# Kernel optimization log

Measured on AMD Instinct MI355X. Metric: run time of the kernel, lower is better.

The kernel has to match this reference:

```python
import jax, jax.numpy as jnp
import numpy as np

B, F, D, K = 4096, 1, 256, 65536

def setup_inputs() -> dict:
    key = jax.random.key(0)
    k1, k2, k3 = jax.random.split(key, 3)
    xhat_BFD = jax.random.normal(k1, (B, F, D), dtype=jnp.float32)
    x_BD = jax.random.normal(k2, (B * F, D), dtype=jnp.float32)
    centroids = jax.random.normal(k3, (K, D), dtype=jnp.float32)
    return {"xhat_BFD": xhat_BFD, "x_BD": x_BD, "centroids": centroids}

def reference(xhat_BFD, x_BD, centroids):
    c_sq_K = jnp.sum(centroids * centroids, axis=-1)            # [K]
    dists_BK = c_sq_K[None, :] - 2.0 * (x_BD @ centroids.T)     # [B*F, K] (GEMM-based distances)
    codes_B = jnp.argmin(dists_BK, axis=-1)                      # [B*F]
    quant_x_BD = centroids[codes_B]                              # embedding lookup of winners
    Bb, Ff, Dd = xhat_BFD.shape
    xhat_next = quant_x_BD.reshape(Bb, Ff, Dd)
    codes_BF = codes_B.reshape(Bb, Ff)
    return xhat_next, codes_BF
```

## Files before the change

kernel.cpp:

```cpp
#include <hip/hip_runtime.h>
#include <hip/hip_bf16.h>
#include <math.h>


#define DDIM 256
#define QTILE 128
#define STSZ 4096
#define QCAP 48
#define F16_MINN 6.103515625e-5f

typedef __attribute__((ext_vector_type(8))) _Float16 half8;
typedef __attribute__((ext_vector_type(4))) _Float16 half4;
typedef __attribute__((ext_vector_type(4))) float f32x4;

__device__ __forceinline__ void gl_lds16(const void* g, void* l) {
  __builtin_amdgcn_global_load_lds((const __attribute__((address_space(1))) void*)g,
                                   (__attribute__((address_space(3))) void*)l, 16, 0, 0);
}

__device__ __forceinline__ unsigned fkey(float d) {
  unsigned ud = __float_as_uint(d);
  return ud ^ (((int)ud < 0) ? 0xFFFFFFFFu : 0x80000000u);
}

__global__ void initctl_kernel(unsigned* __restrict__ ctl) {
  if (threadIdx.x < 64) ctl[threadIdx.x] = 0u;
}

__global__ __launch_bounds__(256) void splitc_kernel(const float* __restrict__ in,
                                                     _Float16* __restrict__ o0,
                                                     float* __restrict__ c_sq) {
  int i = blockIdx.x * 256 + threadIdx.x;
  int lane = (int)threadIdx.x & 63;
  float4 v = ((const float4*)in)[i];
  float vv[4] = {v.x, v.y, v.z, v.w};
  half4 h0;
#pragma unroll
  for (int e = 0; e < 4; ++e)
    h0[e] = (fabsf(vv[e]) < F16_MINN) ? (_Float16)0.f : (_Float16)vv[e];
  *(half4*)(o0 + (size_t)i * 4) = h0;
  float s = fmaf(v.x, v.x, fmaf(v.y, v.y, fmaf(v.z, v.z, v.w * v.w)));
#pragma unroll
  for (int off = 32; off > 0; off >>= 1) s += __shfl_down(s, off, 64);
  if (lane == 0) c_sq[i >> 6] = s;
}

__global__ __launch_bounds__(256) void splitx_kernel(const float* __restrict__ in,
                                                     _Float16* __restrict__ o0, int n4) {
  int i = blockIdx.x * 256 + threadIdx.x;
  if (i >= n4) return;
  float4 v = ((const float4*)in)[i];
  float vv[4] = {v.x, v.y, v.z, v.w};
  half4 h0;
#pragma unroll
  for (int e = 0; e < 4; ++e)
    h0[e] = (fabsf(vv[e]) < F16_MINN) ? (_Float16)0.f : (_Float16)vv[e];
  *(half4*)(o0 + (size_t)i * 4) = h0;
}

__global__ __launch_bounds__(256) void cmax_kernel(const float* __restrict__ c_sq,
                                                   unsigned* __restrict__ ctl) {
  __shared__ float red[4];
  int t = blockIdx.x * 256 + (int)threadIdx.x;
  float4 v = ((const float4*)c_sq)[t];
  float m = fmaxf(fmaxf(v.x, v.y), fmaxf(v.z, v.w));
#pragma unroll
  for (int off = 32; off > 0; off >>= 1) m = fmaxf(m, __shfl_down(m, off, 64));
  int lane = (int)threadIdx.x & 63, w = (int)threadIdx.x >> 6;
  if (lane == 0) red[w] = m;
  __syncthreads();
  if (threadIdx.x == 0) {
    m = fmaxf(fmaxf(red[0], red[1]), fmaxf(red[2], red[3]));
    atomicMax(&ctl[32], __float_as_uint(m));
  }
}

__global__ __launch_bounds__(512, 2) void scan_kernel(
    const _Float16* __restrict__ x0, const _Float16* __restrict__ c0,
    const float* __restrict__ c_sq, float* __restrict__ dm) {
  __shared__ __align__(16) _Float16 As0[32768];

  const int qb = blockIdx.x, kc = blockIdx.y;
  const int tid = (int)threadIdx.x;
  const int lane = tid & 63, w = tid >> 6;
  const int col = lane & 15, quad = lane >> 4;
  const int qrow0 = qb * QTILE;

#pragma unroll
  for (int i = 0; i < 8; ++i) {
    int u = i * 512 + tid;
    int kt = u >> 9, q = (u >> 7) & 3, r = u & 127;
    gl_lds16(x0 + (size_t)(qrow0 + r) * DDIM + kt * 32 + q * 8, As0 + (size_t)u * 8);
  }
  __syncthreads();

  for (int ct = 0; ct < STSZ / 512; ++ct) {
    const int cbase = kc * STSZ + ct * 512 + w * 64;
    f32x4 acc[4][8];
#pragma unroll
    for (int cm = 0; cm < 4; ++cm)
#pragma unroll
      for (int qn = 0; qn < 8; ++qn) acc[cm][qn] = (f32x4)0.0f;

#pragma unroll 2
    for (int kt = 0; kt < 8; ++kt) {
      const int k0 = kt * 32;
      half8 cf[4];
#pragma unroll
      for (int cm = 0; cm < 4; ++cm)
        cf[cm] = *(const half8*)(c0 + (size_t)(cbase + cm * 16 + col) * DDIM + k0 + quad * 8);
#pragma unroll
      for (int qn = 0; qn < 8; ++qn) {
        half8 qf = *(const half8*)(As0 + (((kt * 4 + quad) * QTILE) + qn * 16 + col) * 8);
#pragma unroll
        for (int cm = 0; cm < 4; ++cm)
          acc[cm][qn] = __builtin_amdgcn_mfma_f32_16x16x32_f16(cf[cm], qf, acc[cm][qn], 0, 0, 0);
      }
    }

    f32x4 csv[4];
#pragma unroll
    for (int cm = 0; cm < 4; ++cm)
      csv[cm] = *(const f32x4*)(c_sq + cbase + cm * 16 + quad * 4);
#pragma unroll
    for (int h = 0; h < 2; ++h) {
      const int grp = kc * (STSZ / 32) + ct * 16 + w * 2 + h;
      float* dmg = dm + (size_t)grp * 4096 + qrow0;
#pragma unroll
      for (int qn = 0; qn < 8; ++qn) {
        float mq = INFINITY;
#pragma unroll
        for (int c2 = 0; c2 < 2; ++c2) {
          int cm = h * 2 + c2;
#pragma unroll
          for (int rg = 0; rg < 4; ++rg)
            mq = fminf(mq, fmaf(-2.0f, acc[cm][qn][rg], csv[cm][rg]));
        }
        mq = fminf(mq, __shfl_xor(mq, 16, 64));
        mq = fminf(mq, __shfl_xor(mq, 32, 64));
        if (quad == 0) dmg[qn * 16 + col] = mq;
      }
    }
  }
}

__global__ __launch_bounds__(256) void pmin_kernel(const float* __restrict__ dm,
                                                   float* __restrict__ pm) {
  int qc = blockIdx.x & 15, gc = blockIdx.x >> 4;
  int q = qc * 256 + (int)threadIdx.x;
  float m = INFINITY;
  for (int g = gc * 128; g < gc * 128 + 128; ++g)
    m = fminf(m, dm[(size_t)g * 4096 + q]);
  pm[gc * 4096 + q] = m;
}

__global__ __launch_bounds__(256) void tq_kernel(const float* __restrict__ pm,
                                                 const float* __restrict__ x,
                                                 const unsigned* __restrict__ ctl,
                                                 float* __restrict__ T,
                                                 unsigned* __restrict__ cnt) {
  int q = blockIdx.x * 256 + (int)threadIdx.x;
  float M = INFINITY;
#pragma unroll
  for (int i = 0; i < 16; ++i) M = fminf(M, pm[i * 4096 + q]);
  float xsq = 0.f;
  const float4* xr = (const float4*)(x + (size_t)q * DDIM);
#pragma unroll 8
  for (int i = 0; i < 64; ++i) {
    float4 v = xr[i];
    xsq = fmaf(v.x, v.x, fmaf(v.y, v.y, fmaf(v.z, v.z, fmaf(v.w, v.w, xsq))));
  }
  float cmaxsq = __uint_as_float(ctl[32]);
  T[q] = M + 0.0078125f * sqrtf(xsq * cmaxsq) + 1.0f;
  cnt[q] = 0u;
}

__global__ __launch_bounds__(256) void emit_kernel(const float* __restrict__ dm,
                                                   const float* __restrict__ T,
                                                   unsigned short* __restrict__ cand,
                                                   unsigned* __restrict__ cnt) {
  int qc = blockIdx.x & 15, gc = blockIdx.x >> 4;
  int q = qc * 256 + (int)threadIdx.x;
  float t = T[q];
  for (int g = gc * 128; g < gc * 128 + 128; ++g)
    if (dm[(size_t)g * 4096 + q] <= t) {
      unsigned slot = atomicAdd(&cnt[q], 1u);
      if (slot < QCAP) cand[(size_t)q * QCAP + slot] = (unsigned short)g;
    }
}

__global__ __launch_bounds__(256) void rescore_final_kernel(
    const unsigned short* __restrict__ cand, const unsigned* __restrict__ cnt,
    const float* __restrict__ x, const float* __restrict__ cent,
    const float* __restrict__ c_sq, float* __restrict__ out) {
  int q = blockIdx.x * 4 + ((int)threadIdx.x >> 6);
  int lane = (int)threadIdx.x & 63;
  unsigned n = cnt[q];
  unsigned long long best = 0xFFFFFFFFFFFFFFFFull;
  if (n >= 1 && n <= QCAP) {
    int dh = (lane & 1) * 128;
    const float4* xr = (const float4*)(x + (size_t)q * DDIM + dh);
    for (unsigned sl = 0; sl < n; ++sl) {
      int g = (int)cand[(size_t)q * QCAP + sl];
      int c = g * 32 + (lane >> 1);
      const float4* cr = (const float4*)(cent + (size_t)c * DDIM + dh);
      float s = 0.f;
#pragma unroll
      for (int i = 0; i < 32; ++i) {
        float4 a = xr[i], bb = cr[i];
        s = fmaf(a.x, bb.x, fmaf(a.y, bb.y, fmaf(a.z, bb.z, fmaf(a.w, bb.w, s))));
      }
      s += __shfl_xor(s, 1, 64);
      float d = (lane & 1) ? INFINITY : fmaf(-2.0f, s, c_sq[c]);
      unsigned long long pkv = ((unsigned long long)fkey(d) << 32) | (unsigned)c;
      if (pkv < best) best = pkv;
    }
  } else {
    const float4* xr = (const float4*)(x + (size_t)q * DDIM);
    for (int c = lane; c < 65536; c += 64) {
      const float4* cr = (const float4*)(cent + (size_t)c * DDIM);
      float s = 0.f;
#pragma unroll 16
      for (int i = 0; i < 64; ++i) {
        float4 a = xr[i], bb = cr[i];
        s = fmaf(a.x, bb.x, fmaf(a.y, bb.y, fmaf(a.z, bb.z, fmaf(a.w, bb.w, s))));
      }
      float d = fmaf(-2.0f, s, c_sq[c]);
      unsigned long long pkv = ((unsigned long long)fkey(d) << 32) | (unsigned)c;
      if (pkv < best) best = pkv;
    }
  }
#pragma unroll
  for (int off = 1; off < 64; off <<= 1) {
    unsigned long long o = __shfl_xor(best, off, 64);
    if (o < best) best = o;
  }
  int idx = (int)(unsigned)(best & 0xFFFFFFFFu);
  float4 v = ((const float4*)cent)[(size_t)idx * 64 + lane];
  ((float4*)out)[(size_t)q * 64 + lane] = v;
  if (lane == 0) out[(size_t)4096 * DDIM + q] = (float)idx;
}

extern "C" void kernel_launch(void* const* d_in, const int* in_sizes, int n_in,
                              void* d_out, int out_size, void* d_ws, size_t ws_size,
                              hipStream_t stream) {
  const float* x    = (const float*)d_in[1];
  const float* cent = (const float*)d_in[2];
  float* out = (float*)d_out;
  char* ws = (char*)d_ws;

  const size_t OFF_C0   = 0;
  const size_t OFF_X0   = 33554432;
  const size_t OFF_CSQ  = 35651584;
  const size_t OFF_CTL  = 35913728;
  const size_t OFF_DM   = 35913984;
  const size_t OFF_PM   = 69468416;
  const size_t OFF_T    = 69730560;
  const size_t OFF_CNT  = 69746944;
  const size_t OFF_CAND = 69763328;
  const size_t NEED     = 72089600;
  if (ws_size < NEED) return;

  _Float16* c0 = (_Float16*)(ws + OFF_C0);
  _Float16* x0 = (_Float16*)(ws + OFF_X0);
  float* c_sq = (float*)(ws + OFF_CSQ);
  unsigned* ctl = (unsigned*)(ws + OFF_CTL);
  float* dm = (float*)(ws + OFF_DM);
  float* pm = (float*)(ws + OFF_PM);
  float* T  = (float*)(ws + OFF_T);
  unsigned* cnt = (unsigned*)(ws + OFF_CNT);
  unsigned short* cand = (unsigned short*)(ws + OFF_CAND);

  initctl_kernel<<<1, 64, 0, stream>>>(ctl);
  splitc_kernel<<<16384, 256, 0, stream>>>(cent, c0, c_sq);
  splitx_kernel<<<1024, 256, 0, stream>>>(x, x0, 4096 * 256 / 4);
  cmax_kernel<<<64, 256, 0, stream>>>(c_sq, ctl);
  scan_kernel<<<dim3(32, 16), 512, 0, stream>>>(x0, c0, c_sq, dm);
  pmin_kernel<<<256, 256, 0, stream>>>(dm, pm);
  tq_kernel<<<16, 256, 0, stream>>>(pm, x, ctl, T, cnt);
  emit_kernel<<<256, 256, 0, stream>>>(dm, T, cand, cnt);
  rescore_final_kernel<<<1024, 256, 0, stream>>>(cand, cnt, x, cent, c_sq, out);
}
```

Before: 401.7 us.

## Restructure scan kernel to 32x32x16 MFMA with smaller query tile

```diff
diff --git a/kernel.cpp b/kernel.cpp
--- a/kernel.cpp
+++ b/kernel.cpp
@@ -4,7 +4,7 @@
 
 
 #define DDIM 256
-#define QTILE 128
+#define QTILE 64
 #define STSZ 4096
 #define QCAP 48
 #define F16_MINN 6.103515625e-5f
@@ -12,6 +12,7 @@
 typedef __attribute__((ext_vector_type(8))) _Float16 half8;
 typedef __attribute__((ext_vector_type(4))) _Float16 half4;
 typedef __attribute__((ext_vector_type(4))) float f32x4;
+typedef __attribute__((ext_vector_type(16))) float f32x16;
 
 __device__ __forceinline__ void gl_lds16(const void* g, void* l) {
   __builtin_amdgcn_global_load_lds((const __attribute__((address_space(1))) void*)g,
@@ -75,70 +76,66 @@
   }
 }
 
-__global__ __launch_bounds__(512, 2) void scan_kernel(
+__global__ __launch_bounds__(256, 3) void scan_kernel(
     const _Float16* __restrict__ x0, const _Float16* __restrict__ c0,
     const float* __restrict__ c_sq, float* __restrict__ dm) {
-  __shared__ __align__(16) _Float16 As0[32768];
+  __shared__ __align__(16) _Float16 As0[16384];
 
   const int qb = blockIdx.x, kc = blockIdx.y;
   const int tid = (int)threadIdx.x;
   const int lane = tid & 63, w = tid >> 6;
-  const int col = lane & 15, quad = lane >> 4;
+  const int lo = lane & 31, hi = lane >> 5;
   const int qrow0 = qb * QTILE;
 
 #pragma unroll
   for (int i = 0; i < 8; ++i) {
-    int u = i * 512 + tid;
-    int kt = u >> 9, q = (u >> 7) & 3, r = u & 127;
-    gl_lds16(x0 + (size_t)(qrow0 + r) * DDIM + kt * 32 + q * 8, As0 + (size_t)u * 8);
+    int u = i * 256 + tid;
+    int q = u & 63, s = u >> 6;
+    gl_lds16(x0 + (size_t)(qrow0 + q) * DDIM + s * 8, As0 + (size_t)u * 8);
   }
   __syncthreads();
 
-  for (int ct = 0; ct < STSZ / 512; ++ct) {
-    const int cbase = kc * STSZ + ct * 512 + w * 64;
-    f32x4 acc[4][8];
-#pragma unroll
-    for (int cm = 0; cm < 4; ++cm)
-#pragma unroll
-      for (int qn = 0; qn < 8; ++qn) acc[cm][qn] = (f32x4)0.0f;
-
-#pragma unroll 2
-    for (int kt = 0; kt < 8; ++kt) {
-      const int k0 = kt * 32;
-      half8 cf[4];
-#pragma unroll
-      for (int cm = 0; cm < 4; ++cm)
-        cf[cm] = *(const half8*)(c0 + (size_t)(cbase + cm * 16 + col) * DDIM + k0 + quad * 8);
-#pragma unroll
-      for (int qn = 0; qn < 8; ++qn) {
-        half8 qf = *(const half8*)(As0 + (((kt * 4 + quad) * QTILE) + qn * 16 + col) * 8);
-#pragma unroll
-        for (int cm = 0; cm < 4; ++cm)
-          acc[cm][qn] = __builtin_amdgcn_mfma_f32_16x16x32_f16(cf[cm], qf, acc[cm][qn], 0, 0, 0);
-      }
-    }
-
-    f32x4 csv[4];
-#pragma unroll
-    for (int cm = 0; cm < 4; ++cm)
-      csv[cm] = *(const f32x4*)(c_sq + cbase + cm * 16 + quad * 4);
-#pragma unroll
-    for (int h = 0; h < 2; ++h) {
-      const int grp = kc * (STSZ / 32) + ct * 16 + w * 2 + h;
+  for (int ct = 0; ct < STSZ / 256; ++ct) {
+    const int cbase = kc * STSZ + ct * 256 + w * 64;
+    f32x16 acc[2][2];
+#pragma unroll
+    for (int cm = 0; cm < 2; ++cm)
+#pragma unroll
+      for (int qn = 0; qn < 2; ++qn) acc[cm][qn] = (f32x16)0.0f;
+
+#pragma unroll 4
+    for (int kt = 0; kt < 16; ++kt) {
+      half8 cf[2];
+#pragma unroll
+      for (int cm = 0; cm < 2; ++cm)
+        cf[cm] = *(const half8*)(c0 + (size_t)(cbase + cm * 32 + lo) * DDIM + kt * 16 + hi * 8);
+      half8 qf[2];
+#pragma unroll
+      for (int qn = 0; qn < 2; ++qn)
+        qf[qn] = *(const half8*)(As0 + (size_t)(((kt * 2 + hi) * 64) + qn * 32 + lo) * 8);
+#pragma unroll
+      for (int cm = 0; cm < 2; ++cm)
+#pragma unroll
+        for (int qn = 0; qn < 2; ++qn)
+          acc[cm][qn] = __builtin_amdgcn_mfma_f32_32x32x16_f16(cf[cm], qf[qn], acc[cm][qn], 0, 0, 0);
+    }
+
+#pragma unroll
+    for (int cm = 0; cm < 2; ++cm) {
+      f32x4 csv[4];
+#pragma unroll
+      for (int g = 0; g < 4; ++g)
+        csv[g] = *(const f32x4*)(c_sq + cbase + cm * 32 + g * 8 + hi * 4);
+      const int grp = kc * (STSZ / 32) + ct * 8 + w * 2 + cm;
       float* dmg = dm + (size_t)grp * 4096 + qrow0;
 #pragma unroll
-      for (int qn = 0; qn < 8; ++qn) {
+      for (int qn = 0; qn < 2; ++qn) {
         float mq = INFINITY;
 #pragma unroll
-        for (int c2 = 0; c2 < 2; ++c2) {
-          int cm = h * 2 + c2;
-#pragma unroll
-          for (int rg = 0; rg < 4; ++rg)
-            mq = fminf(mq, fmaf(-2.0f, acc[cm][qn][rg], csv[cm][rg]));
-        }
-        mq = fminf(mq, __shfl_xor(mq, 16, 64));
+        for (int r = 0; r < 16; ++r)
+          mq = fminf(mq, fmaf(-2.0f, acc[cm][qn][r], csv[r >> 2][r & 3]));
         mq = fminf(mq, __shfl_xor(mq, 32, 64));
-        if (quad == 0) dmg[qn * 16 + col] = mq;
+        if (hi == 0) dmg[qn * 32 + lo] = mq;
       }
     }
   }
@@ -275,7 +272,7 @@
   splitc_kernel<<<16384, 256, 0, stream>>>(cent, c0, c_sq);
   splitx_kernel<<<1024, 256, 0, stream>>>(x, x0, 4096 * 256 / 4);
   cmax_kernel<<<64, 256, 0, stream>>>(c_sq, ctl);
-  scan_kernel<<<dim3(32, 16), 512, 0, stream>>>(x0, c0, c_sq, dm);
+  scan_kernel<<<dim3(64, 16), 256, 0, stream>>>(x0, c0, c_sq, dm);
   pmin_kernel<<<256, 256, 0, stream>>>(dm, pm);
   tq_kernel<<<16, 256, 0, stream>>>(pm, x, ctl, T, cnt);
   emit_kernel<<<256, 256, 0, stream>>>(dm, T, cand, cnt);
```

Result: slower. 499.7 us (+24.4%).
